# Kernel optimization log

Measured on AMD Instinct MI355X. Metric: run time of the kernel, lower is better.

The kernel has to match this reference:

```python
import jax, jax.numpy as jnp
import numpy as np

IN_DIM = 4096
HID_DIM = 4096
OUT_DIM = 4096
BATCH = 8192


def setup_inputs() -> dict:
    key = jax.random.key(0)
    k_x, k_w1, k_b1, k_w2, k_b2 = jax.random.split(key, 5)
    s1 = 1.0 / np.sqrt(IN_DIM)
    s2 = 1.0 / np.sqrt(HID_DIM)
    return {
        "x": jax.random.normal(k_x, (BATCH, IN_DIM), dtype=jnp.float32),
        "W1": jax.random.uniform(k_w1, (HID_DIM, IN_DIM), jnp.float32, -s1, s1),
        "b1": jax.random.uniform(k_b1, (HID_DIM,), jnp.float32, -s1, s1),
        "W2": jax.random.uniform(k_w2, (OUT_DIM, HID_DIM), jnp.float32, -s2, s2),
        "b2": jax.random.uniform(k_b2, (OUT_DIM,), jnp.float32, -s2, s2),
    }


def reference(x, W1, b1, W2, b2):
    # fc1 + ReLU: [B, in] @ [in, hid] -> [B, hid]
    h = jax.nn.relu(jnp.einsum("bi,hi->bh", x, W1) + b1)
    # fc2: [B, hid] @ [hid, out] -> [B, out]
    y = jnp.einsum("bh,oh->bo", h, W2) + b2
    # Spike generation: the torch loop over columns is just (y > 0).float(),
    # fused here into a single vectorized threshold.
    spikes = (y > 0).astype(y.dtype)
    return spikes
```

## Files before the change

### kernel.cpp

```cpp
#include <hip/hip_runtime.h>


constexpr int B_TOT = 8192, IN = 4096, HID = 4096, OUT = 4096;
constexpr int BM = 128, BN = 128, BK = 32;
constexpr int KBLK_TILES = 512 / BK;
constexpr int WS_STRIDE = 144;

__device__ __forceinline__ int wb(int c) { return c * 8 + ((c >> 2) & 3) * 4; }

template <bool RELU_STORE>
__global__ __launch_bounds__(256, 2)
void gemm_exact(const float* __restrict__ A, const float* __restrict__ W,
                const float* __restrict__ bias, float* __restrict__ C,
                int N, int K) {
#pragma clang fp contract(off)
  __shared__ float As[BK][BM];
  __shared__ float Ws[BK * WS_STRIDE];

  const int tid = threadIdx.x;
  const int tc = tid & 15;
  const int tr = tid >> 4;
  const int bm = blockIdx.y * BM;
  const int bn = blockIdx.x * BN;

  const int srow = tid >> 1;
  const int kb   = (tid & 1) * 16;
  const int wwb  = wb(srow >> 3) + (srow & 7);

  float tot[8][8], blk[8][8];
#pragma unroll
  for (int i = 0; i < 8; ++i)
#pragma unroll
    for (int j = 0; j < 8; ++j) { tot[i][j] = 0.0f; blk[i][j] = 0.0f; }

  const float* arow = A + (size_t)(bm + srow) * K + kb;
  const float* wrow = W + (size_t)(bn + srow) * K + kb;

  const int NT = K / BK;
  for (int t = 0; t < NT; ++t) {
    float4 av[4], wv[4];
#pragma unroll
    for (int u = 0; u < 4; ++u) {
      av[u] = *reinterpret_cast<const float4*>(arow + t * BK + 4 * u);
      wv[u] = *reinterpret_cast<const float4*>(wrow + t * BK + 4 * u);
    }
    if (t > 0 && (t % KBLK_TILES) == 0) {
#pragma unroll
      for (int i = 0; i < 8; ++i)
#pragma unroll
        for (int j = 0; j < 8; ++j) {
          tot[i][j] = __fadd_rn(tot[i][j], blk[i][j]);
          blk[i][j] = 0.0f;
        }
    }
    __syncthreads();
#pragma unroll
    for (int u = 0; u < 4; ++u) {
      const float va[4] = {av[u].x, av[u].y, av[u].z, av[u].w};
      const float vw[4] = {wv[u].x, wv[u].y, wv[u].z, wv[u].w};
#pragma unroll
      for (int e = 0; e < 4; ++e) {
        const int kk = kb + 4 * u + e;
        As[kk][srow] = va[e];
        Ws[kk * WS_STRIDE + wwb] = vw[e];
      }
    }
    __syncthreads();

#pragma unroll 2
    for (int kk = 0; kk < BK; ++kk) {
      float a[8], w[8];
      *reinterpret_cast<float4*>(&a[0]) =
          *reinterpret_cast<const float4*>(&As[kk][tr * 8]);
      *reinterpret_cast<float4*>(&a[4]) =
          *reinterpret_cast<const float4*>(&As[kk][tr * 8 + 4]);
      const float* wp = &Ws[kk * WS_STRIDE + wb(tc)];
      *reinterpret_cast<float4*>(&w[0]) = *reinterpret_cast<const float4*>(wp);
      *reinterpret_cast<float4*>(&w[4]) = *reinterpret_cast<const float4*>(wp + 4);
#pragma unroll
      for (int i = 0; i < 8; ++i)
#pragma unroll
        for (int j = 0; j < 8; ++j)
          blk[i][j] = __fmaf_rn(a[i], w[j], blk[i][j]);
    }
  }

  float bs[8];
#pragma unroll
  for (int j = 0; j < 8; ++j) bs[j] = bias[bn + tc * 8 + j];
#pragma unroll
  for (int i = 0; i < 8; ++i) {
    const size_t m = (size_t)(bm + tr * 8 + i);
    float o[8];
#pragma unroll
    for (int j = 0; j < 8; ++j) {
      float v = __fadd_rn(tot[i][j], blk[i][j]);
      v = __fadd_rn(v, bs[j]);
      if constexpr (RELU_STORE)
        o[j] = v > 0.0f ? v : 0.0f;
      else
        o[j] = v > 0.0f ? 1.0f : 0.0f;
    }
    float* cp = C + m * N + bn + tc * 8;
    *reinterpret_cast<float4*>(cp)     = make_float4(o[0], o[1], o[2], o[3]);
    *reinterpret_cast<float4*>(cp + 4) = make_float4(o[4], o[5], o[6], o[7]);
  }
}

extern "C" void kernel_launch(void* const* d_in, const int* in_sizes, int n_in,
                              void* d_out, int out_size, void* d_ws, size_t ws_size,
                              hipStream_t stream) {
  const float* x  = (const float*)d_in[0];
  const float* W1 = (const float*)d_in[1];
  const float* b1 = (const float*)d_in[2];
  const float* W2 = (const float*)d_in[3];
  const float* b2 = (const float*)d_in[4];
  float* out = (float*)d_out;

  const dim3 blk(256);

  size_t rows = ws_size / ((size_t)HID * sizeof(float));
  rows = (rows / BM) * BM;
  if (rows > (size_t)B_TOT) rows = B_TOT;
  if (rows < BM) rows = BM;
  float* h = (float*)d_ws;

  for (int m0 = 0; m0 < B_TOT; m0 += (int)rows) {
    const int mrows = (B_TOT - m0 < (int)rows) ? (B_TOT - m0) : (int)rows;
    const dim3 g1(HID / BN, mrows / BM);
    const dim3 g2(OUT / BN, mrows / BM);
    gemm_exact<true><<<g1, blk, 0, stream>>>(
        x + (size_t)m0 * IN, W1, b1, h, HID, IN);
    gemm_exact<false><<<g2, blk, 0, stream>>>(
        h, W2, b2, out + (size_t)m0 * OUT, OUT, HID);
  }
}
```

Baseline: 6.161 ms.

## Widen GEMM tile to 128x256, prefetch through registers, split K into per-launch passes

Each thread's output micro-tile grows from 8x8 to 8x16 (BN=256), which raises reuse of each shared-memory A value. The next K-tile is loaded from global memory into registers while the current tile is computed, which drops one barrier per iteration. The 512-wide K-block accumulation moves out of the kernel into separate kernel launches that keep the running partial sum in a global workspace, so the summation order stays exactly the same. In exchange, every pass reads and writes the full partial matrix through global memory, there are more launches, and the workspace rows are halved because a second partial buffer is needed.

```diff
diff --git a/kernel.cpp b/kernel.cpp
--- a/kernel.cpp
+++ b/kernel.cpp
@@ -2,20 +2,18 @@
 
 
 constexpr int B_TOT = 8192, IN = 4096, HID = 4096, OUT = 4096;
-constexpr int BM = 128, BN = 128, BK = 32;
-constexpr int KBLK_TILES = 512 / BK;
-constexpr int WS_STRIDE = 144;
+constexpr int BM = 128, BN = 256, BK = 32;
+constexpr int KBLK = 512;
+constexpr int NT = KBLK / BK;
 
-__device__ __forceinline__ int wb(int c) { return c * 8 + ((c >> 2) & 3) * 4; }
-
-template <bool RELU_STORE>
+template <int MODE, bool RELU>
 __global__ __launch_bounds__(256, 2)
-void gemm_exact(const float* __restrict__ A, const float* __restrict__ W,
-                const float* __restrict__ bias, float* __restrict__ C,
-                int N, int K) {
+void gemm_pass(const float* __restrict__ A, const float* __restrict__ W,
+               const float* __restrict__ bias, const float* Cprev,
+               float* Cout, int N, int K, int k0) {
 #pragma clang fp contract(off)
   __shared__ float As[BK][BM];
-  __shared__ float Ws[BK * WS_STRIDE];
+  __shared__ float Ws[BK * BN];
 
   const int tid = threadIdx.x;
   const int tc = tid & 15;
@@ -24,86 +22,130 @@
   const int bn = blockIdx.x * BN;
 
   const int srow = tid >> 1;
-  const int kb   = (tid & 1) * 16;
-  const int wwb  = wb(srow >> 3) + (srow & 7);
+  const int kb = (tid & 1) * 16;
+  const int cw = ((tid >> 2) & 3) * 64 + (tid >> 4) * 4 + (tid & 3);
 
-  float tot[8][8], blk[8][8];
+  const float* arow = A + (size_t)(bm + srow) * K + (k0 + kb);
+  const float* wrow = W + (size_t)(bn + tid) * K + k0;
+
+  float4 av[4], wv[8];
+#define PREFETCH(t)                                                        \
+  {                                                                        \
+    _Pragma("unroll") for (int u = 0; u < 4; ++u)                          \
+        av[u] = *reinterpret_cast<const float4*>(arow + (t)*BK + 4 * u);   \
+    _Pragma("unroll") for (int u = 0; u < 8; ++u)                          \
+        wv[u] = *reinterpret_cast<const float4*>(wrow + (t)*BK + 4 * u);   \
+  }
+#define STAGE_WRITE()                                                      \
+  {                                                                        \
+    _Pragma("unroll") for (int u = 0; u < 4; ++u) {                        \
+      const float va[4] = {av[u].x, av[u].y, av[u].z, av[u].w};            \
+      _Pragma("unroll") for (int e = 0; e < 4; ++e)                        \
+          As[kb + 4 * u + e][srow] = va[e];                                \
+    }                                                                      \
+    _Pragma("unroll") for (int u = 0; u < 8; ++u) {                        \
+      const float vw[4] = {wv[u].x, wv[u].y, wv[u].z, wv[u].w};            \
+      _Pragma("unroll") for (int e = 0; e < 4; ++e)                        \
+          Ws[(4 * u + e) * BN + cw] = vw[e];                               \
+    }                                                                      \
+  }
+
+  float blk[8][16];
 #pragma unroll
   for (int i = 0; i < 8; ++i)
 #pragma unroll
-    for (int j = 0; j < 8; ++j) { tot[i][j] = 0.0f; blk[i][j] = 0.0f; }
+    for (int j = 0; j < 16; ++j) blk[i][j] = 0.0f;
 
-  const float* arow = A + (size_t)(bm + srow) * K + kb;
-  const float* wrow = W + (size_t)(bn + srow) * K + kb;
+  PREFETCH(0)
+  STAGE_WRITE()
+  __syncthreads();
 
-  const int NT = K / BK;
   for (int t = 0; t < NT; ++t) {
-    float4 av[4], wv[4];
-#pragma unroll
-    for (int u = 0; u < 4; ++u) {
-      av[u] = *reinterpret_cast<const float4*>(arow + t * BK + 4 * u);
-      wv[u] = *reinterpret_cast<const float4*>(wrow + t * BK + 4 * u);
-    }
-    if (t > 0 && (t % KBLK_TILES) == 0) {
-#pragma unroll
-      for (int i = 0; i < 8; ++i)
-#pragma unroll
-        for (int j = 0; j < 8; ++j) {
-          tot[i][j] = __fadd_rn(tot[i][j], blk[i][j]);
-          blk[i][j] = 0.0f;
-        }
-    }
-    __syncthreads();
-#pragma unroll
-    for (int u = 0; u < 4; ++u) {
-      const float va[4] = {av[u].x, av[u].y, av[u].z, av[u].w};
-      const float vw[4] = {wv[u].x, wv[u].y, wv[u].z, wv[u].w};
-#pragma unroll
-      for (int e = 0; e < 4; ++e) {
-        const int kk = kb + 4 * u + e;
-        As[kk][srow] = va[e];
-        Ws[kk * WS_STRIDE + wwb] = vw[e];
-      }
-    }
-    __syncthreads();
-
+    if (t + 1 < NT) PREFETCH(t + 1)
 #pragma unroll 2
     for (int kk = 0; kk < BK; ++kk) {
-      float a[8], w[8];
+      float a[8], w[16];
       *reinterpret_cast<float4*>(&a[0]) =
           *reinterpret_cast<const float4*>(&As[kk][tr * 8]);
       *reinterpret_cast<float4*>(&a[4]) =
           *reinterpret_cast<const float4*>(&As[kk][tr * 8 + 4]);
-      const float* wp = &Ws[kk * WS_STRIDE + wb(tc)];
-      *reinterpret_cast<float4*>(&w[0]) = *reinterpret_cast<const float4*>(wp);
-      *reinterpret_cast<float4*>(&w[4]) = *reinterpret_cast<const float4*>(wp + 4);
+#pragma unroll
+      for (int q = 0; q < 4; ++q)
+        *reinterpret_cast<float4*>(&w[4 * q]) =
+            *reinterpret_cast<const float4*>(&Ws[kk * BN + q * 64 + tc * 4]);
 #pragma unroll
       for (int i = 0; i < 8; ++i)
 #pragma unroll
-        for (int j = 0; j < 8; ++j)
+        for (int j = 0; j < 16; ++j)
           blk[i][j] = __fmaf_rn(a[i], w[j], blk[i][j]);
     }
+    __syncthreads();
+    if (t + 1 < NT) {
+      STAGE_WRITE()
+      __syncthreads();
+    }
   }
+#undef PREFETCH
+#undef STAGE_WRITE
 
-  float bs[8];
+  float bs[16];
+  if constexpr (MODE == 2) {
 #pragma unroll
-  for (int j = 0; j < 8; ++j) bs[j] = bias[bn + tc * 8 + j];
+    for (int j = 0; j < 16; ++j) bs[j] = bias[bn + tc * 16 + j];
+  }
 #pragma unroll
   for (int i = 0; i < 8; ++i) {
     const size_t m = (size_t)(bm + tr * 8 + i);
-    float o[8];
+    const size_t base = m * N + bn + tc * 16;
+    float4 cv[4];
+    if constexpr (MODE >= 1) {
 #pragma unroll
-    for (int j = 0; j < 8; ++j) {
-      float v = __fadd_rn(tot[i][j], blk[i][j]);
-      v = __fadd_rn(v, bs[j]);
-      if constexpr (RELU_STORE)
-        o[j] = v > 0.0f ? v : 0.0f;
-      else
-        o[j] = v > 0.0f ? 1.0f : 0.0f;
+      for (int q = 0; q < 4; ++q)
+        cv[q] = *reinterpret_cast<const float4*>(Cprev + base + 4 * q);
     }
-    float* cp = C + m * N + bn + tc * 8;
-    *reinterpret_cast<float4*>(cp)     = make_float4(o[0], o[1], o[2], o[3]);
-    *reinterpret_cast<float4*>(cp + 4) = make_float4(o[4], o[5], o[6], o[7]);
+    float o[16];
+#pragma unroll
+    for (int j = 0; j < 16; ++j) {
+      float v = blk[i][j];
+      if constexpr (MODE >= 1) {
+        const float pj = (&cv[j >> 2].x)[j & 3];
+        v = __fadd_rn(pj, v);
+      }
+      if constexpr (MODE == 2) {
+        v = __fadd_rn(v, bs[j]);
+        o[j] = RELU ? (v > 0.0f ? v : 0.0f) : (v > 0.0f ? 1.0f : 0.0f);
+      } else {
+        o[j] = v;
+      }
+    }
+#pragma unroll
+    for (int q = 0; q < 4; ++q)
+      *reinterpret_cast<float4*>(Cout + base + 4 * q) =
+          make_float4(o[4 * q], o[4 * q + 1], o[4 * q + 2], o[4 * q + 3]);
+  }
+}
+
+static void run_layer(const float* A, const float* W, const float* bias,
+                      float* partial, float* dest, bool relu, int rows,
+                      int N, int K, hipStream_t stream) {
+  const dim3 blk(256);
+  const dim3 g(N / BN, rows / BM);
+  const int NP = K / KBLK;
+  for (int p = 0; p < NP; ++p) {
+    const int k0 = p * KBLK;
+    if (p == 0) {
+      gemm_pass<0, false><<<g, blk, 0, stream>>>(A, W, bias, nullptr, partial,
+                                                 N, K, k0);
+    } else if (p < NP - 1) {
+      gemm_pass<1, false><<<g, blk, 0, stream>>>(A, W, bias, partial, partial,
+                                                 N, K, k0);
+    } else if (relu) {
+      gemm_pass<2, true><<<g, blk, 0, stream>>>(A, W, bias, partial, dest,
+                                                N, K, k0);
+    } else {
+      gemm_pass<2, false><<<g, blk, 0, stream>>>(A, W, bias, partial, dest,
+                                                 N, K, k0);
+    }
   }
 }
 
@@ -117,21 +159,18 @@
   const float* b2 = (const float*)d_in[4];
   float* out = (float*)d_out;
 
-  const dim3 blk(256);
-
-  size_t rows = ws_size / ((size_t)HID * sizeof(float));
+  size_t rows = ws_size / ((size_t)2 * HID * sizeof(float));
   rows = (rows / BM) * BM;
   if (rows > (size_t)B_TOT) rows = B_TOT;
   if (rows < BM) rows = BM;
-  float* h = (float*)d_ws;
+
+  float* h   = (float*)d_ws;
+  float* y2p = h + (size_t)rows * HID;
 
   for (int m0 = 0; m0 < B_TOT; m0 += (int)rows) {
     const int mrows = (B_TOT - m0 < (int)rows) ? (B_TOT - m0) : (int)rows;
-    const dim3 g1(HID / BN, mrows / BM);
-    const dim3 g2(OUT / BN, mrows / BM);
-    gemm_exact<true><<<g1, blk, 0, stream>>>(
-        x + (size_t)m0 * IN, W1, b1, h, HID, IN);
-    gemm_exact<false><<<g2, blk, 0, stream>>>(
-        h, W2, b2, out + (size_t)m0 * OUT, OUT, HID);
+    run_layer(x + (size_t)m0 * IN, W1, b1, h, h, true, mrows, HID, IN, stream);
+    run_layer(h, W2, b2, y2p, out + (size_t)m0 * OUT, false, mrows, OUT, HID,
+              stream);
   }
 }
```

After: 6.175 ms. Within noise of the previous version (+0.2%).

## Load A rows via wave-uniform scalar loads and double-buffer W tiles in LDS

Applied to the files above, without the earlier changes.

Restructures the exact-FP32 GEMM so each wave owns 8 rows of A. Those rows are read directly from global memory through wave-uniform (readfirstlane) addresses, so the compiler can use scalar loads, and A is no longer staged in LDS. Only W is staged, in a double-buffered LDS tile of 512 columns by 16 k, with a register prefetch of the next tile that overlaps compute. Tile shape changes to 64x512 with 512 threads and one block per CU. This cuts LDS traffic and barriers but adds many scalar memory loads per k-step and lowers occupancy.

```diff
diff --git a/kernel.cpp b/kernel.cpp
--- a/kernel.cpp
+++ b/kernel.cpp
@@ -2,30 +2,70 @@
 
 
 constexpr int B_TOT = 8192, IN = 4096, HID = 4096, OUT = 4096;
-constexpr int BM = 128, BN = 128, BK = 32;
+constexpr int BM = 64, BN = 512, BK = 16;
+constexpr int WSTR = 512;
 constexpr int KBLK_TILES = 512 / BK;
-constexpr int WS_STRIDE = 144;
 
-__device__ __forceinline__ int wb(int c) { return c * 8 + ((c >> 2) & 3) * 4; }
-
-template <bool RELU_STORE>
-__global__ __launch_bounds__(256, 2)
-void gemm_exact(const float* __restrict__ A, const float* __restrict__ W,
-                const float* __restrict__ bias, float* __restrict__ C,
-                int N, int K) {
+template <bool RELU>
+__global__ __launch_bounds__(512, 1)
+void gemm_sgpr(const float* __restrict__ A, const float* __restrict__ W,
+               const float* __restrict__ bias, float* __restrict__ C,
+               int N, int K) {
 #pragma clang fp contract(off)
-  __shared__ float As[BK][BM];
-  __shared__ float Ws[BK * WS_STRIDE];
+  __shared__ float Ws[2][BK * WSTR];
 
   const int tid = threadIdx.x;
-  const int tc = tid & 15;
-  const int tr = tid >> 4;
+  const int lane = tid & 63;
+  const int wv = __builtin_amdgcn_readfirstlane(tid >> 6);
   const int bm = blockIdx.y * BM;
   const int bn = blockIdx.x * BN;
 
-  const int srow = tid >> 1;
-  const int kb   = (tid & 1) * 16;
-  const int wwb  = wb(srow >> 3) + (srow & 7);
+  const float* Ar[8];
+#pragma unroll
+  for (int i = 0; i < 8; ++i)
+    Ar[i] = A + (size_t)(bm + wv * 8 + i) * K;
+
+  const int cw = (tid >> 3) * 4 + (tid & 3) + ((tid & 4) << 6);
+  const float* wrow = W + (size_t)(bn + tid) * K;
+  const int rb0 = lane * 4;
+  const int rb1 = 256 + lane * 4;
+
+  float4 wv4[4];
+#define PREFETCH(t)                                                         \
+  {                                                                         \
+    _Pragma("unroll") for (int u = 0; u < 4; ++u)                           \
+        wv4[u] = *reinterpret_cast<const float4*>(wrow + (t)*BK + 4 * u);   \
+  }
+#define STAGE_WRITE(B)                                                      \
+  {                                                                         \
+    _Pragma("unroll") for (int u = 0; u < 4; ++u) {                         \
+      const float vw[4] = {wv4[u].x, wv4[u].y, wv4[u].z, wv4[u].w};         \
+      _Pragma("unroll") for (int e = 0; e < 4; ++e)                         \
+          Ws[B][(4 * u + e) * WSTR + cw] = vw[e];                           \
+    }                                                                       \
+  }
+#define COMPUTE(B, t)                                                       \
+  _Pragma("unroll") for (int kk = 0; kk < BK; ++kk) {                       \
+    const int kg = (t)*BK + kk;                                             \
+    float a[8];                                                             \
+    _Pragma("unroll") for (int i = 0; i < 8; ++i) a[i] = Ar[i][kg];         \
+    float w[8];                                                             \
+    *reinterpret_cast<float4*>(&w[0]) =                                     \
+        *reinterpret_cast<const float4*>(&Ws[B][kk * WSTR + rb0]);          \
+    *reinterpret_cast<float4*>(&w[4]) =                                     \
+        *reinterpret_cast<const float4*>(&Ws[B][kk * WSTR + rb1]);          \
+    _Pragma("unroll") for (int i = 0; i < 8; ++i)                           \
+        _Pragma("unroll") for (int j = 0; j < 8; ++j)                       \
+            blk[i][j] = __fmaf_rn(a[i], w[j], blk[i][j]);                   \
+  }
+#define FOLD()                                                              \
+  {                                                                         \
+    _Pragma("unroll") for (int i = 0; i < 8; ++i)                           \
+        _Pragma("unroll") for (int j = 0; j < 8; ++j) {                     \
+      tot[i][j] = __fadd_rn(tot[i][j], blk[i][j]);                          \
+      blk[i][j] = 0.0f;                                                     \
+    }                                                                       \
+  }
 
   float tot[8][8], blk[8][8];
 #pragma unroll
@@ -33,77 +73,52 @@
 #pragma unroll
     for (int j = 0; j < 8; ++j) { tot[i][j] = 0.0f; blk[i][j] = 0.0f; }
 
-  const float* arow = A + (size_t)(bm + srow) * K + kb;
-  const float* wrow = W + (size_t)(bn + srow) * K + kb;
+  const int NT = K / BK;
 
-  const int NT = K / BK;
-  for (int t = 0; t < NT; ++t) {
-    float4 av[4], wv[4];
-#pragma unroll
-    for (int u = 0; u < 4; ++u) {
-      av[u] = *reinterpret_cast<const float4*>(arow + t * BK + 4 * u);
-      wv[u] = *reinterpret_cast<const float4*>(wrow + t * BK + 4 * u);
-    }
-    if (t > 0 && (t % KBLK_TILES) == 0) {
-#pragma unroll
-      for (int i = 0; i < 8; ++i)
-#pragma unroll
-        for (int j = 0; j < 8; ++j) {
-          tot[i][j] = __fadd_rn(tot[i][j], blk[i][j]);
-          blk[i][j] = 0.0f;
-        }
+  PREFETCH(0)
+  STAGE_WRITE(0)
+  PREFETCH(1)
+  __syncthreads();
+
+  for (int t = 0; t < NT; t += 2) {
+    if (t > 0 && (t % KBLK_TILES) == 0) FOLD()
+    COMPUTE(0, t)
+    STAGE_WRITE(1)
+    if (t + 2 < NT) PREFETCH(t + 2)
+    __syncthreads();
+    COMPUTE(1, t + 1)
+    if (t + 2 < NT) {
+      STAGE_WRITE(0)
+      if (t + 3 < NT) PREFETCH(t + 3)
     }
     __syncthreads();
-#pragma unroll
-    for (int u = 0; u < 4; ++u) {
-      const float va[4] = {av[u].x, av[u].y, av[u].z, av[u].w};
-      const float vw[4] = {wv[u].x, wv[u].y, wv[u].z, wv[u].w};
-#pragma unroll
-      for (int e = 0; e < 4; ++e) {
-        const int kk = kb + 4 * u + e;
-        As[kk][srow] = va[e];
-        Ws[kk * WS_STRIDE + wwb] = vw[e];
-      }
-    }
-    __syncthreads();
-
-#pragma unroll 2
-    for (int kk = 0; kk < BK; ++kk) {
-      float a[8], w[8];
-      *reinterpret_cast<float4*>(&a[0]) =
-          *reinterpret_cast<const float4*>(&As[kk][tr * 8]);
-      *reinterpret_cast<float4*>(&a[4]) =
-          *reinterpret_cast<const float4*>(&As[kk][tr * 8 + 4]);
-      const float* wp = &Ws[kk * WS_STRIDE + wb(tc)];
-      *reinterpret_cast<float4*>(&w[0]) = *reinterpret_cast<const float4*>(wp);
-      *reinterpret_cast<float4*>(&w[4]) = *reinterpret_cast<const float4*>(wp + 4);
-#pragma unroll
-      for (int i = 0; i < 8; ++i)
-#pragma unroll
-        for (int j = 0; j < 8; ++j)
-          blk[i][j] = __fmaf_rn(a[i], w[j], blk[i][j]);
-    }
   }
+#undef PREFETCH
+#undef STAGE_WRITE
+#undef COMPUTE
+#undef FOLD
 
   float bs[8];
 #pragma unroll
-  for (int j = 0; j < 8; ++j) bs[j] = bias[bn + tc * 8 + j];
+  for (int q = 0; q < 2; ++q)
+    *reinterpret_cast<float4*>(&bs[4 * q]) =
+        *reinterpret_cast<const float4*>(&bias[bn + lane * 8 + 4 * q]);
 #pragma unroll
   for (int i = 0; i < 8; ++i) {
-    const size_t m = (size_t)(bm + tr * 8 + i);
+    const size_t base = (size_t)(bm + wv * 8 + i) * N + bn + lane * 8;
     float o[8];
 #pragma unroll
     for (int j = 0; j < 8; ++j) {
       float v = __fadd_rn(tot[i][j], blk[i][j]);
       v = __fadd_rn(v, bs[j]);
-      if constexpr (RELU_STORE)
+      if constexpr (RELU)
         o[j] = v > 0.0f ? v : 0.0f;
       else
         o[j] = v > 0.0f ? 1.0f : 0.0f;
     }
-    float* cp = C + m * N + bn + tc * 8;
-    *reinterpret_cast<float4*>(cp)     = make_float4(o[0], o[1], o[2], o[3]);
-    *reinterpret_cast<float4*>(cp + 4) = make_float4(o[4], o[5], o[6], o[7]);
+    *reinterpret_cast<float4*>(C + base) = make_float4(o[0], o[1], o[2], o[3]);
+    *reinterpret_cast<float4*>(C + base + 4) =
+        make_float4(o[4], o[5], o[6], o[7]);
   }
 }
 
@@ -117,7 +132,7 @@
   const float* b2 = (const float*)d_in[4];
   float* out = (float*)d_out;
 
-  const dim3 blk(256);
+  const dim3 blk(512);
 
   size_t rows = ws_size / ((size_t)HID * sizeof(float));
   rows = (rows / BM) * BM;
@@ -129,9 +144,9 @@
     const int mrows = (B_TOT - m0 < (int)rows) ? (B_TOT - m0) : (int)rows;
     const dim3 g1(HID / BN, mrows / BM);
     const dim3 g2(OUT / BN, mrows / BM);
-    gemm_exact<true><<<g1, blk, 0, stream>>>(
+    gemm_sgpr<true><<<g1, blk, 0, stream>>>(
         x + (size_t)m0 * IN, W1, b1, h, HID, IN);
-    gemm_exact<false><<<g2, blk, 0, stream>>>(
+    gemm_sgpr<false><<<g2, blk, 0, stream>>>(
         h, W2, b2, out + (size_t)m0 * OUT, OUT, HID);
   }
 }
```

New measurement: 8.698 ms. 1.41x slower.
